# Kernel tuning notes

Measured on AMD Instinct MI355X. Metric: run time of the kernel, lower is better.

Reference implementation:

```python
import jax, jax.numpy as jnp
import numpy as np

N = 8192      # nodes (= hidden_channels / heads)
E = 262144    # edges (avg degree 32)
IN = 256      # in_channels
H = 8         # heads
C = 32        # out_channels per head
NEG_SLOPE = 0.2


def setup_inputs() -> dict:
    key = jax.random.key(0)
    ks = jax.random.split(key, 8)
    x = jax.random.normal(ks[0], (N, IN), jnp.float32)
    edge_index = jax.random.randint(ks[1], (2, E), 0, N, dtype=jnp.int32)
    lin_w = jax.random.normal(ks[2], (H * C, IN), jnp.float32) * (1.0 / np.sqrt(IN))
    att_src = jax.random.normal(ks[3], (H, C), jnp.float32) * 0.1
    att_dst = jax.random.normal(ks[4], (H, C), jnp.float32) * 0.1
    bias = jax.random.normal(ks[5], (H * C,), jnp.float32) * 0.01
    out_w = jax.random.normal(ks[6], (C, N * H * C), jnp.float32) * (1.0 / np.sqrt(N * H * C))
    out_b = jax.random.normal(ks[7], (C,), jnp.float32) * 0.01
    return {"x": x, "edge_index": edge_index, "lin_w": lin_w, "att_src": att_src,
            "att_dst": att_dst, "bias": bias, "out_w": out_w, "out_b": out_b}


def reference(x, edge_index, lin_w, att_src, att_dst, bias, out_w, out_b):
    n = x.shape[0]
    # PyG GATConv default: add self loops
    loop = jnp.arange(n, dtype=edge_index.dtype)
    src = jnp.concatenate([edge_index[0], loop])  # message sources j
    dst = jnp.concatenate([edge_index[1], loop])  # message targets i
    # per-head linear projection: [n, H, C]
    xh = (x @ lin_w.T).reshape(n, H, C)
    a_src = jnp.einsum('nhc,hc->nh', xh, att_src)  # [n, H]
    a_dst = jnp.einsum('nhc,hc->nh', xh, att_dst)  # [n, H]
    # edge attention logits + segment softmax over incoming edges of each dst
    e = jax.nn.leaky_relu(a_src[src] + a_dst[dst], negative_slope=NEG_SLOPE)  # [E', H]
    m = jax.ops.segment_max(e, dst, num_segments=n)        # [n, H]
    ex = jnp.exp(e - m[dst])
    denom = jax.ops.segment_sum(ex, dst, num_segments=n)   # [n, H]
    alpha = ex / denom[dst]                                 # [E', H]
    # weighted scatter-add aggregation
    agg = jax.ops.segment_sum(alpha[:, :, None] * xh[src], dst, num_segments=n)  # [n, H, C]
    out = agg.reshape(n, H * C) + bias
    # flatten all nodes, dense output layer, softmax
    y = out.reshape(-1) @ out_w.T + out_b  # [C]
    return jax.nn.softmax(y)
```

## Files before the change

### kernel.cpp

```cpp
#include <hip/hip_runtime.h>


namespace {
constexpr int  kN    = 8192;
constexpr int  kE    = 262144;
constexpr int  kTotE = kE + kN;
constexpr long kK    = 2097152;
constexpr int  kYB   = 256;
}

typedef float vfloat4 __attribute__((ext_vector_type(4)));

static __device__ __forceinline__ ushort f2bf(float f) {
  unsigned u = __float_as_uint(f);
  return (ushort)((u + 0x7FFFu + ((u >> 16) & 1u)) >> 16);
}
static __device__ __forceinline__ float bf2f(ushort b) {
  return __uint_as_float(((unsigned)b) << 16);
}

__global__ __launch_bounds__(256) void gemm_xh(const float* __restrict__ x,
                                               const float* __restrict__ lw,
                                               float* __restrict__ xh,
                                               ushort* __restrict__ xh_bf) {
  __shared__ float As[16][68];
  __shared__ float Bs[16][68];
  const int t  = threadIdx.x;
  const int tx = t & 15, ty = t >> 4;
  const int rowBase = blockIdx.x * 64;
  const int colBase = blockIdx.y * 64;
  const int lr = t >> 2;
  const int lk = (t & 3) * 4;

  float acc[4][4] = {};
  for (int kc = 0; kc < 256; kc += 16) {
    float4 av = *(const float4*)(x  + (long)(rowBase + lr) * 256 + kc + lk);
    float4 bv = *(const float4*)(lw + (long)(colBase + lr) * 256 + kc + lk);
    __syncthreads();
    As[lk + 0][lr] = av.x; As[lk + 1][lr] = av.y; As[lk + 2][lr] = av.z; As[lk + 3][lr] = av.w;
    Bs[lk + 0][lr] = bv.x; Bs[lk + 1][lr] = bv.y; Bs[lk + 2][lr] = bv.z; Bs[lk + 3][lr] = bv.w;
    __syncthreads();
#pragma unroll
    for (int k = 0; k < 16; k++) {
      float4 a4 = *(const float4*)(&As[k][ty * 4]);
      float4 b4 = *(const float4*)(&Bs[k][tx * 4]);
      float aa[4] = {a4.x, a4.y, a4.z, a4.w};
      float bb[4] = {b4.x, b4.y, b4.z, b4.w};
#pragma unroll
      for (int i = 0; i < 4; i++)
#pragma unroll
        for (int j = 0; j < 4; j++) acc[i][j] += aa[i] * bb[j];
    }
  }
#pragma unroll
  for (int i = 0; i < 4; i++) {
    const long row = rowBase + ty * 4 + i;
    float4 o = make_float4(acc[i][0], acc[i][1], acc[i][2], acc[i][3]);
    *(float4*)(xh + row * 256 + colBase + tx * 4) = o;
    ushort4 ob = make_ushort4(f2bf(o.x), f2bf(o.y), f2bf(o.z), f2bf(o.w));
    *(ushort4*)(xh_bf + row * 256 + colBase + tx * 4) = ob;
  }
}

__global__ __launch_bounds__(256) void att_deg(const float* __restrict__ xh,
                                               const float* __restrict__ att_s,
                                               const float* __restrict__ att_d,
                                               const int* __restrict__ ei,
                                               float* __restrict__ a_src,
                                               float* __restrict__ a_dst,
                                               int* __restrict__ cnt) {
  const int n = blockIdx.x, t = threadIdx.x;
  float v = xh[(long)n * 256 + t];
  float s = v * att_s[t];
  float d = v * att_d[t];
#pragma unroll
  for (int off = 16; off; off >>= 1) {
    s += __shfl_down(s, off, 32);
    d += __shfl_down(d, off, 32);
  }
  if ((t & 31) == 0) {
    a_src[n * 8 + (t >> 5)] = s;
    a_dst[n * 8 + (t >> 5)] = d;
  }
  const int gid = n * 256 + t;
  if (gid < kE) atomicAdd(&cnt[ei[kE + gid]], 1);
}

__global__ __launch_bounds__(1024) void scan_cnt(const int* __restrict__ cnt,
                                                 int* __restrict__ rowptr,
                                                 int* __restrict__ wpos) {
  __shared__ int s[1024];
  const int t = threadIdx.x;
  int v[8]; int sum = 0;
#pragma unroll
  for (int q = 0; q < 8; q++) { v[q] = cnt[t * 8 + q] + 1; sum += v[q]; }
  s[t] = sum;
  __syncthreads();
  for (int off = 1; off < 1024; off <<= 1) {
    int add = (t >= off) ? s[t - off] : 0;
    __syncthreads();
    s[t] += add;
    __syncthreads();
  }
  int excl = s[t] - sum;
#pragma unroll
  for (int q = 0; q < 8; q++) {
    rowptr[t * 8 + q] = excl;
    wpos[t * 8 + q]   = excl;
    excl += v[q];
  }
  if (t == 1023) rowptr[kN] = s[1023];
}

__global__ __launch_bounds__(256) void scatter_csr(const int* __restrict__ ei,
                                                   const float* __restrict__ a_src,
                                                   const float* __restrict__ a_dst,
                                                   int* __restrict__ wpos,
                                                   int* __restrict__ csr,
                                                   float* __restrict__ w8) {
  int idx = blockIdx.x * 256 + threadIdx.x;
  if (idx >= kTotE) return;
  int s, d;
  if (idx < kE) { s = ei[idx]; d = ei[kE + idx]; }
  else          { s = idx - kE; d = s; }
  int pos = atomicAdd(&wpos[d], 1);
  csr[pos] = s;
  float4 s0 = *(const float4*)(a_src + s * 8);
  float4 s1 = *(const float4*)(a_src + s * 8 + 4);
  float4 d0 = *(const float4*)(a_dst + d * 8);
  float4 d1 = *(const float4*)(a_dst + d * 8 + 4);
  float e[8] = {s0.x + d0.x, s0.y + d0.y, s0.z + d0.z, s0.w + d0.w,
                s1.x + d1.x, s1.y + d1.y, s1.z + d1.z, s1.w + d1.w};
  float w[8];
#pragma unroll
  for (int h = 0; h < 8; h++) {
    float ee = (e[h] > 0.f) ? e[h] : 0.2f * e[h];
    w[h] = __expf(ee);
  }
  float4* wp = (float4*)(w8 + (long)pos * 8);
  wp[0] = make_float4(w[0], w[1], w[2], w[3]);
  wp[1] = make_float4(w[4], w[5], w[6], w[7]);
}

__global__ __launch_bounds__(256) void agg_dot(const ushort* __restrict__ xb,
                                               const float* __restrict__ w8,
                                               const int* __restrict__ rowptr,
                                               const int* __restrict__ csr,
                                               const float* __restrict__ bias,
                                               const float* __restrict__ w,
                                               float* __restrict__ ypart) {
  const int i = blockIdx.x, t = threadIdx.x, h = t >> 5;
  const int lane = t & 63, wid = t >> 6;

  const long wbase = (long)i * 256 + lane * 4;
  vfloat4 wv[8];
#pragma unroll
  for (int cc = 0; cc < 8; cc++) {
    const int c = cc * 4 + wid;
    wv[cc] = __builtin_nontemporal_load((const vfloat4*)(w + (long)c * kK + wbase));
  }

  const int beg = rowptr[i], end = rowptr[i + 1];
  float acc = 0.f, den = 0.f;
  int j = beg;
  for (; j + 8 <= end; j += 8) {
    int   s[8]; float ww[8]; float f[8];
#pragma unroll
    for (int q = 0; q < 8; q++) s[q] = csr[j + q];
#pragma unroll
    for (int q = 0; q < 8; q++) ww[q] = w8[(long)(j + q) * 8 + h];
#pragma unroll
    for (int q = 0; q < 8; q++) f[q] = bf2f(xb[(long)s[q] * 256 + t]);
#pragma unroll
    for (int q = 0; q < 8; q++) { den += ww[q]; acc += ww[q] * f[q]; }
  }
  for (; j < end; j++) {
    int s0 = csr[j];
    float w0 = w8[(long)j * 8 + h];
    den += w0;
    acc += w0 * bf2f(xb[(long)s0 * 256 + t]);
  }

  __shared__ float ofs[256];
  __shared__ float yb[32];
  ofs[t] = acc / den + bias[t];
  __syncthreads();
  float4 f4 = *(const float4*)(ofs + lane * 4);
#pragma unroll
  for (int cc = 0; cc < 8; cc++) {
    float p = wv[cc].x * f4.x + wv[cc].y * f4.y + wv[cc].z * f4.z + wv[cc].w * f4.w;
    p += __shfl_down(p, 32, 64);
    p += __shfl_down(p, 16, 64);
    p += __shfl_down(p, 8, 64);
    p += __shfl_down(p, 4, 64);
    p += __shfl_down(p, 2, 64);
    p += __shfl_down(p, 1, 64);
    if (lane == 0) yb[cc * 4 + wid] = p;
  }
  __syncthreads();
  if (t < 32) atomicAdd(&ypart[(i & (kYB - 1)) * 32 + t], yb[t]);
}

__global__ __launch_bounds__(1024) void finalize(const float* __restrict__ ypart,
                                                 const float* __restrict__ ob,
                                                 float* __restrict__ out) {
  __shared__ float s[32][33];
  const int t = threadIdx.x;
  const int c = t & 31, r = t >> 5;
  float sum = 0.f;
  for (int q = r; q < kYB; q += 32) sum += ypart[q * 32 + c];
  s[c][r] = sum;
  __syncthreads();
  if (t < 32) {
    float y = ob[t];
#pragma unroll
    for (int r2 = 0; r2 < 32; r2++) y += s[t][r2];
    float m = y;
#pragma unroll
    for (int off = 16; off; off >>= 1) m = fmaxf(m, __shfl_xor(m, off, 32));
    float e = __expf(y - m);
    float d = e;
#pragma unroll
    for (int off = 16; off; off >>= 1) d += __shfl_xor(d, off, 32);
    out[t] = e / d;
  }
}

extern "C" void kernel_launch(void* const* d_in, const int* in_sizes, int n_in,
                              void* d_out, int out_size, void* d_ws, size_t ws_size,
                              hipStream_t stream) {
  (void)in_sizes; (void)n_in; (void)out_size; (void)ws_size;
  const float* x     = (const float*)d_in[0];
  const int*   ei    = (const int*)  d_in[1];
  const float* lin_w = (const float*)d_in[2];
  const float* att_s = (const float*)d_in[3];
  const float* att_d = (const float*)d_in[4];
  const float* bias  = (const float*)d_in[5];
  const float* out_w = (const float*)d_in[6];
  const float* out_b = (const float*)d_in[7];
  float* out = (float*)d_out;

  float*  xh       = (float*)d_ws;
  float*  a_src    = xh + kK;
  float*  a_dst    = a_src + kN * 8;
  float*  w8       = a_dst + kN * 8;
  ushort* xh_bf    = (ushort*)(w8 + (long)kTotE * 8);
  int*    cnt      = (int*)(xh_bf + kK);
  float*  ypart    = (float*)(cnt + kN);
  int*    rowptr   = (int*)(ypart + kYB * 32);
  int*    wpos     = rowptr + (kN + 1);
  int*    csr      = wpos + kN;

  (void)hipMemsetAsync(cnt, 0, kN * sizeof(int) + kYB * 32 * sizeof(float), stream);
  gemm_xh    <<<dim3(128, 4), 256, 0, stream>>>(x, lin_w, xh, xh_bf);
  att_deg    <<<kN, 256, 0, stream>>>(xh, att_s, att_d, ei, a_src, a_dst, cnt);
  scan_cnt   <<<1, 1024, 0, stream>>>(cnt, rowptr, wpos);
  scatter_csr<<<(kTotE + 255) / 256, 256, 0, stream>>>(ei, a_src, a_dst, wpos, csr, w8);
  agg_dot    <<<kN, 256, 0, stream>>>(xh_bf, w8, rowptr, csr, bias, out_w, ypart);
  finalize   <<<1, 1024, 0, stream>>>(ypart, out_b, out);
}
```

Baseline: 432.6 us.

## Fuse attention logits and degree histogram into GEMM epilogue; warp-shuffle scan

Folds the attention dot products and the in-degree histogram into the projection GEMM. The GEMM epilogue computes a_src/a_dst directly from register accumulators with 8-lane shuffles, and each GEMM block does two edge-count atomics. This removes the att_deg launch and the fp32 xh write and re-read, keeping only the bf16 copy. The single-block scan now uses wavefront shuffle scans plus a small shared-memory pass instead of a barrier-heavy Hillis-Steele loop. The trade-off is that GEMM blocks now issue atomics before the main loop, which may delay its start.

```diff
diff --git a/kernel.cpp b/kernel.cpp
--- a/kernel.cpp
+++ b/kernel.cpp
@@ -19,10 +19,15 @@
   return __uint_as_float(((unsigned)b) << 16);
 }
 
-__global__ __launch_bounds__(256) void gemm_xh(const float* __restrict__ x,
-                                               const float* __restrict__ lw,
-                                               float* __restrict__ xh,
-                                               ushort* __restrict__ xh_bf) {
+__global__ __launch_bounds__(256) void gemm_att_hist(const float* __restrict__ x,
+                                                     const float* __restrict__ lw,
+                                                     const float* __restrict__ att_s,
+                                                     const float* __restrict__ att_d,
+                                                     const int* __restrict__ ei,
+                                                     ushort* __restrict__ xh_bf,
+                                                     float* __restrict__ a_src,
+                                                     float* __restrict__ a_dst,
+                                                     int* __restrict__ cnt) {
   __shared__ float As[16][68];
   __shared__ float Bs[16][68];
   const int t  = threadIdx.x;
@@ -32,6 +37,13 @@
   const int lr = t >> 2;
   const int lk = (t & 3) * 4;
 
+  {
+    const int bid = blockIdx.y * 128 + blockIdx.x;
+    const int gid = bid * 512 + t;
+    atomicAdd(&cnt[ei[kE + gid]], 1);
+    atomicAdd(&cnt[ei[kE + gid + 256]], 1);
+  }
+
   float acc[4][4] = {};
   for (int kc = 0; kc < 256; kc += 16) {
     float4 av = *(const float4*)(x  + (long)(rowBase + lr) * 256 + kc + lk);
@@ -52,64 +64,69 @@
         for (int j = 0; j < 4; j++) acc[i][j] += aa[i] * bb[j];
     }
   }
+
 #pragma unroll
   for (int i = 0; i < 4; i++) {
     const long row = rowBase + ty * 4 + i;
-    float4 o = make_float4(acc[i][0], acc[i][1], acc[i][2], acc[i][3]);
-    *(float4*)(xh + row * 256 + colBase + tx * 4) = o;
-    ushort4 ob = make_ushort4(f2bf(o.x), f2bf(o.y), f2bf(o.z), f2bf(o.w));
+    ushort4 ob = make_ushort4(f2bf(acc[i][0]), f2bf(acc[i][1]),
+                              f2bf(acc[i][2]), f2bf(acc[i][3]));
     *(ushort4*)(xh_bf + row * 256 + colBase + tx * 4) = ob;
   }
-}
-
-__global__ __launch_bounds__(256) void att_deg(const float* __restrict__ xh,
-                                               const float* __restrict__ att_s,
-                                               const float* __restrict__ att_d,
-                                               const int* __restrict__ ei,
-                                               float* __restrict__ a_src,
-                                               float* __restrict__ a_dst,
-                                               int* __restrict__ cnt) {
-  const int n = blockIdx.x, t = threadIdx.x;
-  float v = xh[(long)n * 256 + t];
-  float s = v * att_s[t];
-  float d = v * att_d[t];
-#pragma unroll
-  for (int off = 16; off; off >>= 1) {
-    s += __shfl_down(s, off, 32);
-    d += __shfl_down(d, off, 32);
-  }
-  if ((t & 31) == 0) {
-    a_src[n * 8 + (t >> 5)] = s;
-    a_dst[n * 8 + (t >> 5)] = d;
-  }
-  const int gid = n * 256 + t;
-  if (gid < kE) atomicAdd(&cnt[ei[kE + gid]], 1);
+
+  float4 as4 = *(const float4*)(att_s + colBase + tx * 4);
+  float4 ad4 = *(const float4*)(att_d + colBase + tx * 4);
+#pragma unroll
+  for (int i = 0; i < 4; i++) {
+    float s = acc[i][0] * as4.x + acc[i][1] * as4.y + acc[i][2] * as4.z + acc[i][3] * as4.w;
+    float d = acc[i][0] * ad4.x + acc[i][1] * ad4.y + acc[i][2] * ad4.z + acc[i][3] * ad4.w;
+#pragma unroll
+    for (int off = 4; off; off >>= 1) {
+      s += __shfl_down(s, off, 8);
+      d += __shfl_down(d, off, 8);
+    }
+    if ((tx & 7) == 0) {
+      const int row  = rowBase + ty * 4 + i;
+      const int head = blockIdx.y * 2 + (tx >> 3);
+      a_src[row * 8 + head] = s;
+      a_dst[row * 8 + head] = d;
+    }
+  }
 }
 
 __global__ __launch_bounds__(1024) void scan_cnt(const int* __restrict__ cnt,
                                                  int* __restrict__ rowptr,
                                                  int* __restrict__ wpos) {
-  __shared__ int s[1024];
-  const int t = threadIdx.x;
+  __shared__ int wsum[16];
+  const int t = threadIdx.x, lane = t & 63, w = t >> 6;
   int v[8]; int sum = 0;
 #pragma unroll
   for (int q = 0; q < 8; q++) { v[q] = cnt[t * 8 + q] + 1; sum += v[q]; }
-  s[t] = sum;
-  __syncthreads();
-  for (int off = 1; off < 1024; off <<= 1) {
-    int add = (t >= off) ? s[t - off] : 0;
-    __syncthreads();
-    s[t] += add;
-    __syncthreads();
-  }
-  int excl = s[t] - sum;
+  int sc = sum;
+#pragma unroll
+  for (int off = 1; off < 64; off <<= 1) {
+    int n = __shfl_up(sc, off, 64);
+    if (lane >= off) sc += n;
+  }
+  if (lane == 63) wsum[w] = sc;
+  __syncthreads();
+  if (t < 16) {
+    int ws = wsum[t];
+#pragma unroll
+    for (int off = 1; off < 16; off <<= 1) {
+      int n = __shfl_up(ws, off, 16);
+      if ((t & 15) >= off) ws += n;
+    }
+    wsum[t] = ws;
+  }
+  __syncthreads();
+  int excl = (w ? wsum[w - 1] : 0) + sc - sum;
 #pragma unroll
   for (int q = 0; q < 8; q++) {
     rowptr[t * 8 + q] = excl;
     wpos[t * 8 + q]   = excl;
     excl += v[q];
   }
-  if (t == 1023) rowptr[kN] = s[1023];
+  if (t == 1023) rowptr[kN] = excl;
 }
 
 __global__ __launch_bounds__(256) void scatter_csr(const int* __restrict__ ei,
@@ -240,8 +257,7 @@
   const float* out_b = (const float*)d_in[7];
   float* out = (float*)d_out;
 
-  float*  xh       = (float*)d_ws;
-  float*  a_src    = xh + kK;
+  float*  a_src    = (float*)d_ws;
   float*  a_dst    = a_src + kN * 8;
   float*  w8       = a_dst + kN * 8;
   ushort* xh_bf    = (ushort*)(w8 + (long)kTotE * 8);
@@ -252,8 +268,8 @@
   int*    csr      = wpos + kN;
 
   (void)hipMemsetAsync(cnt, 0, kN * sizeof(int) + kYB * 32 * sizeof(float), stream);
-  gemm_xh    <<<dim3(128, 4), 256, 0, stream>>>(x, lin_w, xh, xh_bf);
-  att_deg    <<<kN, 256, 0, stream>>>(xh, att_s, att_d, ei, a_src, a_dst, cnt);
+  gemm_att_hist<<<dim3(128, 4), 256, 0, stream>>>(x, lin_w, att_s, att_d, ei,
+                                                  xh_bf, a_src, a_dst, cnt);
   scan_cnt   <<<1, 1024, 0, stream>>>(cnt, rowptr, wpos);
   scatter_csr<<<(kTotE + 255) / 256, 256, 0, stream>>>(ei, a_src, a_dst, wpos, csr, w8);
   agg_dot    <<<kN, 256, 0, stream>>>(xh_bf, w8, rowptr, csr, bias, out_w, ypart);
```

Result: no change. 427.0 us (-1.3%).
